# Kernel optimization log

Measured on AMD Instinct MI355X. Metric: run time of the kernel, lower is better.

The kernel has to match this reference:

```python
import jax, jax.numpy as jnp
import numpy as np

N_NODES = 50000
N_EDGES = 800000
T_STEPS = 12
IN_CH = 2
HID = 64
OUT_CH = 1


def setup_inputs() -> dict:
    key = jax.random.key(0)
    ks = jax.random.split(key, 10)
    x = jax.random.normal(ks[0], (N_NODES, T_STEPS, IN_CH), dtype=jnp.float32)
    edge_index = jax.random.randint(ks[1], (2, N_EDGES), 0, N_NODES, dtype=jnp.int64)
    # GCNConv params (PyG: out = aggregate(norm * (x @ W)) + b)
    W_gcn = jax.random.normal(ks[2], (IN_CH, HID), dtype=jnp.float32) / np.sqrt(IN_CH)
    b_gcn = jnp.zeros((HID,), dtype=jnp.float32)
    # torch.nn.GRU params (1 layer): weight_ih_l0 [3H, H_in], weight_hh_l0 [3H, H]
    s = 1.0 / np.sqrt(HID)
    W_ih = jax.random.uniform(ks[3], (3 * HID, HID), dtype=jnp.float32, minval=-s, maxval=s)
    W_hh = jax.random.uniform(ks[4], (3 * HID, HID), dtype=jnp.float32, minval=-s, maxval=s)
    b_ih = jax.random.uniform(ks[5], (3 * HID,), dtype=jnp.float32, minval=-s, maxval=s)
    b_hh = jax.random.uniform(ks[6], (3 * HID,), dtype=jnp.float32, minval=-s, maxval=s)
    # Linear head
    W_fc = jax.random.uniform(ks[7], (OUT_CH, HID), dtype=jnp.float32, minval=-s, maxval=s)
    b_fc = jax.random.uniform(ks[8], (OUT_CH,), dtype=jnp.float32, minval=-s, maxval=s)
    return {"x": x, "edge_index": edge_index, "W_gcn": W_gcn, "b_gcn": b_gcn,
            "W_ih": W_ih, "W_hh": W_hh, "b_ih": b_ih, "b_hh": b_hh,
            "W_fc": W_fc, "b_fc": b_fc}


def _gcn_norm(edge_index, num_nodes):
    # PyG gcn_norm with self-loops: deg counts incoming edges + self-loop
    src, dst = edge_index[0], edge_index[1]
    deg = jax.ops.segment_sum(jnp.ones_like(dst, dtype=jnp.float32), dst,
                              num_segments=num_nodes) + 1.0  # self-loop
    dinv = jax.lax.rsqrt(deg)
    edge_norm = dinv[src] * dinv[dst]       # [E]
    self_norm = dinv * dinv                 # [N], self-loop weight
    return src, dst, edge_norm, self_norm


def reference(x, edge_index, W_gcn, b_gcn, W_ih, W_hh, b_ih, b_hh, W_fc, b_fc):
    N, T, _ = x.shape
    src, dst, edge_norm, self_norm = _gcn_norm(edge_index, N)

    def gcn(x_t):  # [N, F_in] -> [N, H]
        h = x_t @ W_gcn                                           # [N, H]
        agg = jax.ops.segment_sum(edge_norm[:, None] * h[src], dst,
                                  num_segments=N)                 # gather-scatter
        agg = agg + self_norm[:, None] * h                        # self-loop term
        return jax.nn.relu(agg + b_gcn)

    # small fixed loop over T timesteps (matches original per-timestep GCN)
    spatial = jnp.stack([gcn(x[:, t, :]) for t in range(T)], axis=0)  # [T, N, H]

    H = W_hh.shape[1]
    def gru_step(h, x_t):
        gi = x_t @ W_ih.T + b_ih        # [N, 3H]
        gh = h @ W_hh.T + b_hh          # [N, 3H]
        i_r, i_z, i_n = gi[:, :H], gi[:, H:2 * H], gi[:, 2 * H:]
        h_r, h_z, h_n = gh[:, :H], gh[:, H:2 * H], gh[:, 2 * H:]
        r = jax.nn.sigmoid(i_r + h_r)
        z = jax.nn.sigmoid(i_z + h_z)
        n = jnp.tanh(i_n + r * h_n)
        h_new = (1.0 - z) * n + z * h
        return h_new, None

    h0 = jnp.zeros((N, H), dtype=x.dtype)
    final_rep, _ = jax.lax.scan(gru_step, h0, spatial)  # last hidden state [N, H]
    predictions = final_rep @ W_fc.T + b_fc             # [N, 1]
    return jnp.squeeze(predictions)                     # [N]
```

## Files before the change

### kernel.cpp

```cpp
#include <hip/hip_runtime.h>
#include <hip/hip_fp16.h>
#include <math.h>

#define T_STEPS 12
#define HID 64
#define GWPB 13
#define GBLOCK (GWPB*64)
#define HSTR2 68
#define B_LDS_BYTES 49152
#define WG_LDS_BYTES 1792
#define H_LDS_BYTES (GWPB*16*HSTR2*4)
#define LDS_TOTAL (B_LDS_BYTES + WG_LDS_BYTES + H_LDS_BYTES)

typedef _Float16 half8 __attribute__((ext_vector_type(8)));
typedef __fp16   fp16x2 __attribute__((ext_vector_type(2)));
typedef __attribute__((ext_vector_type(4))) float floatx4;

__device__ __forceinline__ float fast_sigmoid(float x){
  float e = __builtin_amdgcn_exp2f(-1.442695041f * x);
  return __builtin_amdgcn_rcpf(1.0f + e);
}
__device__ __forceinline__ float fast_tanh(float x){
  float e = __builtin_amdgcn_exp2f(2.885390082f * x);
  return fmaf(-2.0f, __builtin_amdgcn_rcpf(1.0f + e), 1.0f);
}
__device__ __forceinline__ void split2(float f0, float f1, unsigned &hi, unsigned &lo){
  fp16x2 h = __builtin_amdgcn_cvt_pkrtz(f0, f1);
  float b0 = (float)h[0], b1 = (float)h[1];
  fp16x2 l = __builtin_amdgcn_cvt_pkrtz(f0 - b0, f1 - b1);
  hi = __builtin_bit_cast(unsigned, h);
  lo = __builtin_bit_cast(unsigned, l);
}

__global__ void count_packB_kernel(const int* __restrict__ ei, int E, int* __restrict__ cnt,
                                   int* __restrict__ rank,
                                   const float* __restrict__ W_ih, const float* __restrict__ W_hh,
                                   unsigned short* __restrict__ Bpk){
  int tid = blockIdx.x*blockDim.x + threadIdx.x;
  if (tid < E) rank[tid] = atomicAdd(&cnt[ei[E + tid]], 1);
  if (tid < 48*512){
    int q = tid >> 9;
    int rr = tid & 511;
    int l = rr >> 3, j = rr & 7;
    int g, c4, kt;
    if (q < 32){ g = q >> 4; int rem = q & 15; c4 = rem >> 2; kt = rem & 3; }
    else if (q < 40){ g = 2; c4 = (q-32) >> 1; kt = (q-32) & 1; }
    else            { g = 3; c4 = (q-40) >> 1; kt = ((q-40) & 1) + 2; }
    int k  = kt*32 + (l >> 4)*8 + j;
    int n  = l & 15;
    int jc = c4*16 + n;
    float w;
    if (g == 0)      w = (k < 64) ? W_ih[jc*64 + k]      : W_hh[jc*64 + (k-64)];
    else if (g == 1) w = (k < 64) ? W_ih[(64+jc)*64 + k] : W_hh[(64+jc)*64 + (k-64)];
    else if (g == 2) w = W_ih[(128+jc)*64 + k];
    else             w = W_hh[(128+jc)*64 + (k-64)];
    _Float16 hv = (_Float16)w;
    Bpk[q*512 + l*8 + j] = __builtin_bit_cast(unsigned short, hv);
  }
}

__global__ void scan1_kernel(const int* __restrict__ cnt, int* __restrict__ part,
                             int* __restrict__ bsum, int N){
  __shared__ int wsum[16];
  int tid = threadIdx.x;
  int g = blockIdx.x*1024 + tid;
  int v = (g < N) ? cnt[g] : 0;
  int lane = tid & 63, wv = tid >> 6;
  int s = v;
  #pragma unroll
  for (int off = 1; off < 64; off <<= 1){
    int u = __shfl_up(s, off, 64);
    if (lane >= off) s += u;
  }
  if (lane == 63) wsum[wv] = s;
  __syncthreads();
  if (wv == 0){
    int w = (lane < 16) ? wsum[lane] : 0;
    #pragma unroll
    for (int off = 1; off < 16; off <<= 1){
      int u = __shfl_up(w, off, 64);
      if (lane >= off) w += u;
    }
    if (lane < 16) wsum[lane] = w;
  }
  __syncthreads();
  int incl = (wv ? wsum[wv-1] : 0) + s;
  if (g < N) part[g] = incl;
  if (tid == 1023) bsum[blockIdx.x] = incl;
}

__global__ void scan3_kernel(const int* __restrict__ part, const int* __restrict__ bsum,
                             const int* __restrict__ cnt, int* __restrict__ row_start,
                             const float* __restrict__ x, float* __restrict__ dinv,
                             float4* __restrict__ xs, int N, int nb){
  __shared__ int sb[64];
  if (threadIdx.x < 64){
    int v = (threadIdx.x < nb) ? bsum[threadIdx.x] : 0;
    #pragma unroll
    for (int off = 1; off < 64; off <<= 1){
      int u = __shfl_up(v, off, 64);
      if ((int)(threadIdx.x & 63) >= off) v += u;
    }
    sb[threadIdx.x] = v;
  }
  __syncthreads();
  int g = blockIdx.x*blockDim.x + threadIdx.x;
  if (g < N){
    int c = cnt[g];
    int b = g >> 10;
    int incl = part[g] + (b ? sb[b-1] : 0);
    row_start[g] = incl - c;
    if (g == N-1) row_start[N] = incl;
    float dn = rsqrtf((float)c + 1.0f);
    dinv[g] = dn;
    const float4* xg = (const float4*)x + (size_t)g*6;
    float4* xo = xs + (size_t)g*6;
    #pragma unroll
    for (int q = 0; q < 6; ++q){
      float4 v4 = xg[q];
      xo[q] = make_float4(dn*v4.x, dn*v4.y, dn*v4.z, dn*v4.w);
    }
  }
}

__global__ void fill_kernel(const int* __restrict__ ei, int E,
                            const int* __restrict__ row_start,
                            const int* __restrict__ rank, int* __restrict__ csr){
  int e = blockIdx.x*blockDim.x + threadIdx.x;
  if (e < E){
    int dst = ei[E + e];
    csr[row_start[dst] + rank[e]] = ei[e];
  }
}

__global__ void gather6_kernel(const float4* __restrict__ xs, const int* __restrict__ row_start,
                               const int* __restrict__ csr, const float* __restrict__ dinv,
                               float4* __restrict__ rin, int N){
  int tid = blockIdx.x*blockDim.x + threadIdx.x;
  if (tid >= N*12) return;
  int pq  = tid >> 1;
  int par = tid & 1;
  int n = pq / 6;
  int q = pq - n*6;
  int s0 = row_start[n], s1 = row_start[n+1];
  float4 acc = make_float4(0.f, 0.f, 0.f, 0.f);
  int e = s0 + par;
  for (; e + 2 < s1; e += 4){
    float4 va = xs[csr[e]*6 + q];
    float4 vb = xs[csr[e+2]*6 + q];
    acc.x += va.x + vb.x;
    acc.y += va.y + vb.y;
    acc.z += va.z + vb.z;
    acc.w += va.w + vb.w;
  }
  if (e < s1){
    float4 va = xs[csr[e]*6 + q];
    acc.x += va.x; acc.y += va.y; acc.z += va.z; acc.w += va.w;
  }
  acc.x += __shfl_xor(acc.x, 1, 64);
  acc.y += __shfl_xor(acc.y, 1, 64);
  acc.z += __shfl_xor(acc.z, 1, 64);
  acc.w += __shfl_xor(acc.w, 1, 64);
  if (par == 0){
    float4 self = xs[n*6 + q];
    float dn = dinv[n];
    rin[pq] = make_float4(dn*(acc.x + self.x), dn*(acc.y + self.y),
                          dn*(acc.z + self.z), dn*(acc.w + self.w));
  }
}

__global__ __attribute__((amdgpu_waves_per_eu(1, 4))) __launch_bounds__(GBLOCK)
void gru16_kernel(const float* __restrict__ rin,
                  const float* __restrict__ W_gcn, const float* __restrict__ b_gcn,
                  const unsigned short* __restrict__ Bpk,
                  const float* __restrict__ b_ih, const float* __restrict__ b_hh,
                  const float* __restrict__ W_fc, const float* __restrict__ b_fc,
                  float* __restrict__ out, int N, int ntiles){
  extern __shared__ char smem[];
  unsigned short* Bl = (unsigned short*)smem;
  float*    wgl = (float*)(smem + B_LDS_BYTES);
  float*    hl  = (float*)(smem + B_LDS_BYTES + WG_LDS_BYTES);

  {
    const int4* Bg = (const int4*)Bpk;
    int4* Bd = (int4*)smem;
    for (int i = threadIdx.x; i < 3072; i += GBLOCK) Bd[i] = Bg[i];
    if (threadIdx.x < 64){
      int l = threadIdx.x;
      wgl[l]       = W_gcn[l];
      wgl[64 + l]  = W_gcn[64 + l];
      wgl[128 + l] = b_gcn[l];
      wgl[192 + 4*l + 0] = b_ih[l]       + b_hh[l];
      wgl[192 + 4*l + 1] = b_ih[64 + l]  + b_hh[64 + l];
      wgl[192 + 4*l + 2] = b_ih[128 + l];
      wgl[192 + 4*l + 3] = b_hh[128 + l];
    }
  }
  __syncthreads();

  int lane = threadIdx.x & 63;
  int wid  = threadIdx.x >> 6;
  int tile = blockIdx.x*GWPB + wid;
  if (tile >= ntiles) return;
  int n0   = tile << 4;
  int quad = lane >> 4;
  int n16  = lane & 15;
  float* hwp = hl + wid*(16*HSTR2);

  for (int i = lane; i < 16*HSTR2; i += 64) hwp[i] = 0.f;

  float wfc = W_fc[lane], bfc = b_fc[0];

  int nn = n0 + n16; if (nn > N-1) nn = N-1;
  const float* rbase = rin + (size_t)nn*24;
  float2 rcur = *(const float2*)rbase;

  #pragma unroll 1
  for (int t = 0; t < T_STEPS; ++t){
    float2 rnx = (t < T_STEPS-1) ? *(const float2*)(rbase + 2*(t+1)) : rcur;

    half8 ahi[4], alo[4];
    #pragma unroll
    for (int kt = 0; kt < 2; ++kt){
      int j0 = kt*32 + quad*8;
      floatx4 g0a = *(floatx4*)&wgl[j0],       g0b = *(floatx4*)&wgl[j0+4];
      floatx4 g1a = *(floatx4*)&wgl[64 + j0],  g1b = *(floatx4*)&wgl[64 + j0+4];
      floatx4 bga = *(floatx4*)&wgl[128 + j0], bgb = *(floatx4*)&wgl[128 + j0+4];
      float f[8];
      #pragma unroll
      for (int j = 0; j < 4; ++j){
        f[j]   = fmaxf(fmaf(rcur.x, g0a[j], fmaf(rcur.y, g1a[j], bga[j])), 0.f);
        f[4+j] = fmaxf(fmaf(rcur.x, g0b[j], fmaf(rcur.y, g1b[j], bgb[j])), 0.f);
      }
      union { half8 v; unsigned w[4]; } H, L;
      #pragma unroll
      for (int p2 = 0; p2 < 4; ++p2)
        split2(f[2*p2], f[2*p2+1], H.w[p2], L.w[p2]);
      ahi[kt] = H.v; alo[kt] = L.v;
    }
    #pragma unroll
    for (int kt = 2; kt < 4; ++kt){
      int base = n16*HSTR2 + (kt-2)*32 + quad*8;
      floatx4 fa = *(const floatx4*)&hwp[base];
      floatx4 fb = *(const floatx4*)&hwp[base+4];
      union { half8 v; unsigned w[4]; } H, L;
      split2(fa[0], fa[1], H.w[0], L.w[0]);
      split2(fa[2], fa[3], H.w[1], L.w[1]);
      split2(fb[0], fb[1], H.w[2], L.w[2]);
      split2(fb[2], fb[3], H.w[3], L.w[3]);
      ahi[kt] = H.v; alo[kt] = L.v;
    }

    #pragma unroll 2
    for (int c4 = 0; c4 < 4; ++c4){
      int jc = (c4<<4) + n16;
      floatx4 bv = *(floatx4*)&wgl[192 + 4*jc];
      float hpw[4];
      #pragma unroll
      for (int r = 0; r < 4; ++r)
        hpw[r] = hwp[(quad*4 + r)*HSTR2 + (c4<<4) + n16];
      floatx4 aR = (floatx4){bv[0], bv[0], bv[0], bv[0]};
      floatx4 aZ = (floatx4){bv[1], bv[1], bv[1], bv[1]};
      floatx4 aN = (floatx4){bv[2], bv[2], bv[2], bv[2]};
      floatx4 aH = (floatx4){bv[3], bv[3], bv[3], bv[3]};
      #pragma unroll
      for (int kt = 0; kt < 4; ++kt){
        int qr = (c4<<2) + kt;
        half8 wR = *(const half8*)&Bl[qr*512 + lane*8];
        aR = __builtin_amdgcn_mfma_f32_16x16x32_f16(ahi[kt], wR, aR, 0,0,0);
        aR = __builtin_amdgcn_mfma_f32_16x16x32_f16(alo[kt], wR, aR, 0,0,0);
        int qz = 16 + (c4<<2) + kt;
        half8 wZ = *(const half8*)&Bl[qz*512 + lane*8];
        aZ = __builtin_amdgcn_mfma_f32_16x16x32_f16(ahi[kt], wZ, aZ, 0,0,0);
        aZ = __builtin_amdgcn_mfma_f32_16x16x32_f16(alo[kt], wZ, aZ, 0,0,0);
        if (kt < 2){
          int qn = 32 + (c4<<1) + kt;
          half8 wN = *(const half8*)&Bl[qn*512 + lane*8];
          aN = __builtin_amdgcn_mfma_f32_16x16x32_f16(ahi[kt], wN, aN, 0,0,0);
          aN = __builtin_amdgcn_mfma_f32_16x16x32_f16(alo[kt], wN, aN, 0,0,0);
        } else {
          int qh = 40 + (c4<<1) + (kt-2);
          half8 wH = *(const half8*)&Bl[qh*512 + lane*8];
          aH = __builtin_amdgcn_mfma_f32_16x16x32_f16(ahi[kt], wH, aH, 0,0,0);
          aH = __builtin_amdgcn_mfma_f32_16x16x32_f16(alo[kt], wH, aH, 0,0,0);
        }
      }
      #pragma unroll
      for (int r = 0; r < 4; ++r){
        float hprev = hpw[r];
        float rg = fast_sigmoid(aR[r]);
        float zg = fast_sigmoid(aZ[r]);
        float ng = fast_tanh(fmaf(rg, aH[r], aN[r]));
        float hn = fmaf(zg, hprev - ng, ng);
        hwp[(quad*4 + r)*HSTR2 + (c4<<4) + n16] = hn;
      }
    }
    rcur = rnx;
  }

  #pragma unroll 1
  for (int m = 0; m < 16; ++m){
    float hv = hwp[m*HSTR2 + lane];
    float v = hv * wfc;
    #pragma unroll
    for (int off = 32; off >= 1; off >>= 1) v += __shfl_xor(v, off, 64);
    int n = n0 + m;
    if (lane == 0 && n < N) out[n] = v + bfc;
  }
}

extern "C" void kernel_launch(void* const* d_in, const int* in_sizes, int n_in,
                              void* d_out, int out_size, void* d_ws, size_t ws_size,
                              hipStream_t stream){
  const float* x     = (const float*)d_in[0];
  const int*   ei    = (const int*)d_in[1];
  const float* W_gcn = (const float*)d_in[2];
  const float* b_gcn = (const float*)d_in[3];
  const float* W_ih  = (const float*)d_in[4];
  const float* W_hh  = (const float*)d_in[5];
  const float* b_ih  = (const float*)d_in[6];
  const float* b_hh  = (const float*)d_in[7];
  const float* W_fc  = (const float*)d_in[8];
  const float* b_fc  = (const float*)d_in[9];
  float* out = (float*)d_out;
  const int N = in_sizes[0] / (T_STEPS*2);
  const int E = in_sizes[1] / 2;
  const int NB1024 = (N + 1023) / 1024;

  char* p = (char*)d_ws;
  auto alloc = [&](size_t bytes)->char*{
    char* r = p; p += (bytes + 255) & ~(size_t)255; return r;
  };
  int*   cnt       = (int*)  alloc((size_t)N*4);
  int*   row_start = (int*)  alloc((size_t)(N+1)*4);
  int*   rank      = (int*)  alloc((size_t)E*4);
  int*   csr       = (int*)  alloc((size_t)E*4);
  float* dinv      = (float*)alloc((size_t)N*4);
  int*   part      = (int*)  alloc((size_t)N*4);
  int*   bsum      = (int*)  alloc((size_t)NB1024*4);
  float* rin       = (float*)alloc((size_t)N*24*4);
  float* xs        = (float*)alloc((size_t)N*24*4);
  unsigned short* Bpk = (unsigned short*)alloc((size_t)24576*2);

  hipMemsetAsync(cnt, 0, (size_t)N*4, stream);
  {
    int work = (E > 48*512) ? E : 48*512;
    count_packB_kernel<<<(work+255)/256, 256, 0, stream>>>(ei, E, cnt, rank, W_ih, W_hh, Bpk);
  }
  scan1_kernel<<<NB1024, 1024, 0, stream>>>(cnt, part, bsum, N);
  scan3_kernel<<<(N+255)/256, 256, 0, stream>>>(part, bsum, cnt, row_start,
                                                x, dinv, (float4*)xs, N, NB1024);
  fill_kernel<<<(E+255)/256, 256, 0, stream>>>(ei, E, row_start, rank, csr);
  gather6_kernel<<<(N*12+255)/256, 256, 0, stream>>>((const float4*)xs, row_start, csr,
                                                     dinv, (float4*)rin, N);

  (void)hipFuncSetAttribute((const void*)gru16_kernel,
                            hipFuncAttributeMaxDynamicSharedMemorySize, LDS_TOTAL);
  int ntiles = (N + 15) / 16;
  int blocks = (ntiles + GWPB - 1) / GWPB;
  gru16_kernel<<<blocks, GBLOCK, LDS_TOTAL, stream>>>(rin, W_gcn, b_gcn, Bpk,
                                                      b_ih, b_hh, W_fc, b_fc,
                                                      out, N, ntiles);
}
```

Before: 227.3 us.

## Split each GRU tile across two waves sharing hidden state in LDS

Each 16-node tile is now handled by a pair of waves, each computing half of the hidden columns, with the hidden state shared in LDS and block-wide barriers around each timestep's read and write. Blocks hold 7 tiles (14 waves), which halves the per-block hidden-state LDS and doubles the wave count, and the waves-per-EU hint is raised to 8. The goal is more latency hiding and parallelism in the serial recurrence. The cost is that every wave still splits all four A fragments, so that conversion work is duplicated, and two __syncthreads per timestep now couple all waves in a block.

```diff
diff --git a/kernel.cpp b/kernel.cpp
--- a/kernel.cpp
+++ b/kernel.cpp
@@ -4,12 +4,13 @@
 
 #define T_STEPS 12
 #define HID 64
-#define GWPB 13
+#define TPB 7
+#define GWPB (TPB*2)
 #define GBLOCK (GWPB*64)
 #define HSTR2 68
 #define B_LDS_BYTES 49152
 #define WG_LDS_BYTES 1792
-#define H_LDS_BYTES (GWPB*16*HSTR2*4)
+#define H_LDS_BYTES (TPB*16*HSTR2*4)
 #define LDS_TOTAL (B_LDS_BYTES + WG_LDS_BYTES + H_LDS_BYTES)
 
 typedef _Float16 half8 __attribute__((ext_vector_type(8)));
@@ -169,7 +170,7 @@
   }
 }
 
-__global__ __attribute__((amdgpu_waves_per_eu(1, 4))) __launch_bounds__(GBLOCK)
+__global__ __attribute__((amdgpu_waves_per_eu(1, 8))) __launch_bounds__(GBLOCK)
 void gru16_kernel(const float* __restrict__ rin,
                   const float* __restrict__ W_gcn, const float* __restrict__ b_gcn,
                   const unsigned short* __restrict__ Bpk,
@@ -196,18 +197,20 @@
       wgl[192 + 4*l + 3] = b_hh[128 + l];
     }
   }
-  __syncthreads();
 
   int lane = threadIdx.x & 63;
   int wid  = threadIdx.x >> 6;
-  int tile = blockIdx.x*GWPB + wid;
-  if (tile >= ntiles) return;
+  int pairIdx = wid >> 1;
+  int wsub    = wid & 1;
+  int tile0 = blockIdx.x*TPB + pairIdx;
+  int tile  = (tile0 < ntiles) ? tile0 : (ntiles - 1);
   int n0   = tile << 4;
   int quad = lane >> 4;
   int n16  = lane & 15;
-  float* hwp = hl + wid*(16*HSTR2);
+  float* hwp = hl + pairIdx*(16*HSTR2);
 
   for (int i = lane; i < 16*HSTR2; i += 64) hwp[i] = 0.f;
+  __syncthreads();
 
   float wfc = W_fc[lane], bfc = b_fc[0];
 
@@ -250,15 +253,23 @@
       split2(fb[2], fb[3], H.w[3], L.w[3]);
       ahi[kt] = H.v; alo[kt] = L.v;
     }
-
-    #pragma unroll 2
-    for (int c4 = 0; c4 < 4; ++c4){
+    float hpwA[4], hpwB[4];
+    {
+      int c4a = wsub*2, c4b = wsub*2 + 1;
+      #pragma unroll
+      for (int r = 0; r < 4; ++r){
+        hpwA[r] = hwp[(quad*4 + r)*HSTR2 + (c4a<<4) + n16];
+        hpwB[r] = hwp[(quad*4 + r)*HSTR2 + (c4b<<4) + n16];
+      }
+    }
+
+    __syncthreads();
+
+    #pragma unroll
+    for (int cc = 0; cc < 2; ++cc){
+      int c4 = wsub*2 + cc;
       int jc = (c4<<4) + n16;
       floatx4 bv = *(floatx4*)&wgl[192 + 4*jc];
-      float hpw[4];
-      #pragma unroll
-      for (int r = 0; r < 4; ++r)
-        hpw[r] = hwp[(quad*4 + r)*HSTR2 + (c4<<4) + n16];
       floatx4 aR = (floatx4){bv[0], bv[0], bv[0], bv[0]};
       floatx4 aZ = (floatx4){bv[1], bv[1], bv[1], bv[1]};
       floatx4 aN = (floatx4){bv[2], bv[2], bv[2], bv[2]};
@@ -287,7 +298,7 @@
       }
       #pragma unroll
       for (int r = 0; r < 4; ++r){
-        float hprev = hpw[r];
+        float hprev = cc ? hpwB[r] : hpwA[r];
         float rg = fast_sigmoid(aR[r]);
         float zg = fast_sigmoid(aZ[r]);
         float ng = fast_tanh(fmaf(rg, aH[r], aN[r]));
@@ -295,11 +306,14 @@
         hwp[(quad*4 + r)*HSTR2 + (c4<<4) + n16] = hn;
       }
     }
+
+    __syncthreads();
     rcur = rnx;
   }
 
   #pragma unroll 1
-  for (int m = 0; m < 16; ++m){
+  for (int mm = 0; mm < 8; ++mm){
+    int m = wsub*8 + mm;
     float hv = hwp[m*HSTR2 + lane];
     float v = hv * wfc;
     #pragma unroll
@@ -357,7 +371,7 @@
   (void)hipFuncSetAttribute((const void*)gru16_kernel,
                             hipFuncAttributeMaxDynamicSharedMemorySize, LDS_TOTAL);
   int ntiles = (N + 15) / 16;
-  int blocks = (ntiles + GWPB - 1) / GWPB;
+  int blocks = (ntiles + TPB - 1) / TPB;
   gru16_kernel<<<blocks, GBLOCK, LDS_TOTAL, stream>>>(rin, W_gcn, b_gcn, Bpk,
                                                       b_ih, b_hh, W_fc, b_fc,
                                                       out, N, ntiles);
```

Result: slower. 252.3 us (+11.0%).

## Build CSR via two-level bucket radix sort instead of global atomic counting

Applied to the files above, without the earlier changes.

Replaces the per-edge global atomic degree count, rank array and scattered CSR fill with a two-pass counting sort. Destinations are first bucketed by node>>6 using per-block LDS histograms, scanned, and scattered into (src,dst) pairs, then sorted within each 64-node bucket in LDS. The aim is to remove contended global atomics and random global writes, at the cost of extra kernels and an intermediate 8-byte-per-edge buffer. The x scaling moves into its own kernel.

```diff
diff --git a/kernel.cpp b/kernel.cpp
--- a/kernel.cpp
+++ b/kernel.cpp
@@ -12,6 +12,8 @@
 #define H_LDS_BYTES (GWPB*16*HSTR2*4)
 #define LDS_TOTAL (B_LDS_BYTES + WG_LDS_BYTES + H_LDS_BYTES)
 
+#define GRID_P 256
+
 typedef _Float16 half8 __attribute__((ext_vector_type(8)));
 typedef __fp16   fp16x2 __attribute__((ext_vector_type(2)));
 typedef __attribute__((ext_vector_type(4))) float floatx4;
@@ -32,15 +34,28 @@
   lo = __builtin_bit_cast(unsigned, l);
 }
 
-__global__ void count_packB_kernel(const int* __restrict__ ei, int E, int* __restrict__ cnt,
-                                   int* __restrict__ rank,
+
+__global__ void histA_packB_kernel(const int* __restrict__ ei, int E, int nbkt,
+                                   int* __restrict__ table,
                                    const float* __restrict__ W_ih, const float* __restrict__ W_hh,
                                    unsigned short* __restrict__ Bpk){
-  int tid = blockIdx.x*blockDim.x + threadIdx.x;
-  if (tid < E) rank[tid] = atomicAdd(&cnt[ei[E + tid]], 1);
-  if (tid < 48*512){
-    int q = tid >> 9;
-    int rr = tid & 511;
+  __shared__ int h[1024];
+  int tid = threadIdx.x;
+  #pragma unroll
+  for (int i = tid; i < 1024; i += 256) h[i] = 0;
+  __syncthreads();
+  int epb = (E + GRID_P - 1)/GRID_P;
+  int e0 = blockIdx.x*epb, e1 = (e0 + epb < E) ? e0 + epb : E;
+  for (int e = e0 + tid; e < e1; e += 256)
+    atomicAdd(&h[ei[E + e] >> 6], 1);
+  __syncthreads();
+  for (int b = tid; b < nbkt; b += 256)
+    table[b*GRID_P + blockIdx.x] = h[b];
+
+  int gtid = blockIdx.x*256 + tid;
+  if (gtid < 48*512){
+    int q = gtid >> 9;
+    int rr = gtid & 511;
     int l = rr >> 3, j = rr & 7;
     int g, c4, kt;
     if (q < 32){ g = q >> 4; int rem = q & 15; c4 = rem >> 2; kt = rem & 3; }
@@ -60,11 +75,11 @@
 }
 
 __global__ void scan1_kernel(const int* __restrict__ cnt, int* __restrict__ part,
-                             int* __restrict__ bsum, int N){
+                             int* __restrict__ bsum, int Ntot){
   __shared__ int wsum[16];
   int tid = threadIdx.x;
   int g = blockIdx.x*1024 + tid;
-  int v = (g < N) ? cnt[g] : 0;
+  int v = (g < Ntot) ? cnt[g] : 0;
   int lane = tid & 63, wv = tid >> 6;
   int s = v;
   #pragma unroll
@@ -85,52 +100,109 @@
   }
   __syncthreads();
   int incl = (wv ? wsum[wv-1] : 0) + s;
-  if (g < N) part[g] = incl;
+  if (g < Ntot) part[g] = incl;
   if (tid == 1023) bsum[blockIdx.x] = incl;
 }
 
-__global__ void scan3_kernel(const int* __restrict__ part, const int* __restrict__ bsum,
-                             const int* __restrict__ cnt, int* __restrict__ row_start,
-                             const float* __restrict__ x, float* __restrict__ dinv,
-                             float4* __restrict__ xs, int N, int nb){
-  __shared__ int sb[64];
-  if (threadIdx.x < 64){
-    int v = (threadIdx.x < nb) ? bsum[threadIdx.x] : 0;
+__global__ void scan2b_kernel(const int* __restrict__ bsum, int* __restrict__ bincl, int nb){
+  __shared__ int ws4[4];
+  int tid = threadIdx.x;
+  int lane = tid & 63, wv = tid >> 6;
+  int v = (tid < nb) ? bsum[tid] : 0;
+  int s = v;
+  #pragma unroll
+  for (int off = 1; off < 64; off <<= 1){
+    int u = __shfl_up(s, off, 64);
+    if (lane >= off) s += u;
+  }
+  if (lane == 63) ws4[wv] = s;
+  __syncthreads();
+  if (wv == 0){
+    int w = (lane < 4) ? ws4[lane] : 0;
+    #pragma unroll
+    for (int off = 1; off < 4; off <<= 1){
+      int u = __shfl_up(w, off, 64);
+      if (lane >= off) w += u;
+    }
+    if (lane < 4) ws4[lane] = w;
+  }
+  __syncthreads();
+  int incl = (wv ? ws4[wv-1] : 0) + s;
+  if (tid < nb) bincl[tid] = incl;
+}
+
+__device__ __forceinline__ int full_incl(const int* part, const int* bincl, int i){
+  return part[i] + ((i >= 1024) ? bincl[(i >> 10) - 1] : 0);
+}
+
+__global__ void scatterC_kernel(const int* __restrict__ ei, int E, int nbkt,
+                                const int* __restrict__ table,
+                                const int* __restrict__ part, const int* __restrict__ bincl,
+                                int2* __restrict__ sorted){
+  __shared__ int cursor[1024];
+  int tid = threadIdx.x;
+  for (int b = tid; b < nbkt; b += 256){
+    int flat = b*GRID_P + blockIdx.x;
+    cursor[b] = full_incl(part, bincl, flat) - table[flat];
+  }
+  __syncthreads();
+  int epb = (E + GRID_P - 1)/GRID_P;
+  int e0 = blockIdx.x*epb, e1 = (e0 + epb < E) ? e0 + epb : E;
+  for (int e = e0 + tid; e < e1; e += 256){
+    int src = ei[e], dst = ei[E + e];
+    int pos = atomicAdd(&cursor[dst >> 6], 1);
+    sorted[pos] = make_int2(src, dst);
+  }
+}
+
+__global__ void fineD_kernel(const int2* __restrict__ sorted,
+                             const int* __restrict__ part, const int* __restrict__ bincl,
+                             int* __restrict__ row_start, float* __restrict__ dinv,
+                             int* __restrict__ csr, int N, int nbkt){
+  __shared__ int fh[64];
+  __shared__ int fx[64];
+  int tid = threadIdx.x;
+  int b = blockIdx.x;
+  int start = (b == 0) ? 0 : full_incl(part, bincl, b*GRID_P - 1);
+  int end   = full_incl(part, bincl, (b+1)*GRID_P - 1);
+  if (tid < 64) fh[tid] = 0;
+  __syncthreads();
+  for (int i = start + tid; i < end; i += 256)
+    atomicAdd(&fh[sorted[i].y & 63], 1);
+  __syncthreads();
+  if (tid < 64){
+    int c = fh[tid];
+    int s = c;
     #pragma unroll
     for (int off = 1; off < 64; off <<= 1){
-      int u = __shfl_up(v, off, 64);
-      if ((int)(threadIdx.x & 63) >= off) v += u;
-    }
-    sb[threadIdx.x] = v;
-  }
-  __syncthreads();
-  int g = blockIdx.x*blockDim.x + threadIdx.x;
-  if (g < N){
-    int c = cnt[g];
-    int b = g >> 10;
-    int incl = part[g] + (b ? sb[b-1] : 0);
-    row_start[g] = incl - c;
-    if (g == N-1) row_start[N] = incl;
-    float dn = rsqrtf((float)c + 1.0f);
-    dinv[g] = dn;
-    const float4* xg = (const float4*)x + (size_t)g*6;
-    float4* xo = xs + (size_t)g*6;
-    #pragma unroll
-    for (int q = 0; q < 6; ++q){
-      float4 v4 = xg[q];
-      xo[q] = make_float4(dn*v4.x, dn*v4.y, dn*v4.z, dn*v4.w);
-    }
-  }
-}
-
-__global__ void fill_kernel(const int* __restrict__ ei, int E,
-                            const int* __restrict__ row_start,
-                            const int* __restrict__ rank, int* __restrict__ csr){
-  int e = blockIdx.x*blockDim.x + threadIdx.x;
-  if (e < E){
-    int dst = ei[E + e];
-    csr[row_start[dst] + rank[e]] = ei[e];
-  }
+      int u = __shfl_up(s, off, 64);
+      if (tid >= off) s += u;
+    }
+    int excl = s - c;
+    fx[tid] = start + excl;
+    int node = b*64 + tid;
+    if (node < N){
+      row_start[node] = start + excl;
+      dinv[node] = rsqrtf((float)c + 1.0f);
+    }
+    if (b == nbkt-1 && tid == 0) row_start[N] = end;
+  }
+  __syncthreads();
+  for (int i = start + tid; i < end; i += 256){
+    int2 sd = sorted[i];
+    int pos = atomicAdd(&fx[sd.y & 63], 1);
+    csr[pos] = sd.x;
+  }
+}
+
+__global__ void xs_scale_kernel(const float* __restrict__ dinv, const float* __restrict__ x,
+                                float4* __restrict__ xs, int N){
+  int tid = blockIdx.x*blockDim.x + threadIdx.x;
+  if (tid >= N*6) return;
+  int n = tid / 6;
+  float dn = dinv[n];
+  float4 v = ((const float4*)x)[tid];
+  xs[tid] = make_float4(dn*v.x, dn*v.y, dn*v.z, dn*v.w);
 }
 
 __global__ void gather6_kernel(const float4* __restrict__ xs, const int* __restrict__ row_start,
@@ -325,32 +397,32 @@
   float* out = (float*)d_out;
   const int N = in_sizes[0] / (T_STEPS*2);
   const int E = in_sizes[1] / 2;
-  const int NB1024 = (N + 1023) / 1024;
+  const int NBKT = (N + 63) >> 6;
+  const int FLAT = NBKT * GRID_P;
+  const int NB1024 = (FLAT + 1023) / 1024;
 
   char* p = (char*)d_ws;
   auto alloc = [&](size_t bytes)->char*{
     char* r = p; p += (bytes + 255) & ~(size_t)255; return r;
   };
-  int*   cnt       = (int*)  alloc((size_t)N*4);
+  int*   table     = (int*)  alloc((size_t)FLAT*4);
+  int*   part      = (int*)  alloc((size_t)FLAT*4);
+  int*   bsum      = (int*)  alloc((size_t)NB1024*4);
+  int*   bincl     = (int*)  alloc((size_t)NB1024*4);
+  int2*  sorted    = (int2*) alloc((size_t)E*8);
   int*   row_start = (int*)  alloc((size_t)(N+1)*4);
-  int*   rank      = (int*)  alloc((size_t)E*4);
   int*   csr       = (int*)  alloc((size_t)E*4);
   float* dinv      = (float*)alloc((size_t)N*4);
-  int*   part      = (int*)  alloc((size_t)N*4);
-  int*   bsum      = (int*)  alloc((size_t)NB1024*4);
   float* rin       = (float*)alloc((size_t)N*24*4);
   float* xs        = (float*)alloc((size_t)N*24*4);
   unsigned short* Bpk = (unsigned short*)alloc((size_t)24576*2);
 
-  hipMemsetAsync(cnt, 0, (size_t)N*4, stream);
-  {
-    int work = (E > 48*512) ? E : 48*512;
-    count_packB_kernel<<<(work+255)/256, 256, 0, stream>>>(ei, E, cnt, rank, W_ih, W_hh, Bpk);
-  }
-  scan1_kernel<<<NB1024, 1024, 0, stream>>>(cnt, part, bsum, N);
-  scan3_kernel<<<(N+255)/256, 256, 0, stream>>>(part, bsum, cnt, row_start,
-                                                x, dinv, (float4*)xs, N, NB1024);
-  fill_kernel<<<(E+255)/256, 256, 0, stream>>>(ei, E, row_start, rank, csr);
+  histA_packB_kernel<<<GRID_P, 256, 0, stream>>>(ei, E, NBKT, table, W_ih, W_hh, Bpk);
+  scan1_kernel<<<NB1024, 1024, 0, stream>>>(table, part, bsum, FLAT);
+  scan2b_kernel<<<1, 256, 0, stream>>>(bsum, bincl, NB1024);
+  scatterC_kernel<<<GRID_P, 256, 0, stream>>>(ei, E, NBKT, table, part, bincl, sorted);
+  fineD_kernel<<<NBKT, 256, 0, stream>>>(sorted, part, bincl, row_start, dinv, csr, N, NBKT);
+  xs_scale_kernel<<<(N*6+255)/256, 256, 0, stream>>>(dinv, x, (float4*)xs, N);
   gather6_kernel<<<(N*12+255)/256, 256, 0, stream>>>((const float4*)xs, row_start, csr,
                                                      dinv, (float4*)rin, N);
 
```

Result: faster. 205.9 us (-9.4%).
